# Performance work log

Measured on AMD Instinct MI355X. Metric: run time of the kernel, lower is better.

## Reference

```python
import jax, jax.numpy as jnp
import numpy as np

B, S, N, D = 4, 1024, 16, 512
H, HD = 8, 64
THETA = 10000.0


def setup_inputs() -> dict:
    key = jax.random.key(0)
    k0, k1, k2, k3 = jax.random.split(key, 4)
    x = jax.random.normal(k0, (B, S, N, D), dtype=jnp.float32)
    pos_bias = jax.random.normal(k1, (H, N, N), dtype=jnp.float32)
    W_qkv = jax.random.normal(k2, (D, 3 * H * HD), dtype=jnp.float32) / np.sqrt(D).astype(np.float32)
    W_out = jax.random.normal(k3, (H * HD, D), dtype=jnp.float32) / np.sqrt(H * HD).astype(np.float32)
    # mixed mask (not all True -> no early-return path; not all False -> masking active)
    focus_present_mask = jnp.array([True, False, True, False])
    return {"x": x, "pos_bias": pos_bias, "W_qkv": W_qkv, "W_out": W_out,
            "focus_present_mask": focus_present_mask}


def _rotary_cos_sin(n, d, dtype):
    # rotary-embedding-torch: inv_freq over even indices, each freq repeated twice adjacently
    inv_freq = 1.0 / (THETA ** (jnp.arange(0, d, 2, dtype=jnp.float32) / d))
    freqs = jnp.arange(n, dtype=jnp.float32)[:, None] * inv_freq  # (n, d/2)
    freqs = jnp.repeat(freqs, 2, axis=-1)                          # (n, d)
    return jnp.cos(freqs).astype(dtype), jnp.sin(freqs).astype(dtype)


def _rotate_half(t):
    # pairs (x0, x1) -> (-x1, x0), interleaved layout
    t2 = t.reshape(*t.shape[:-1], t.shape[-1] // 2, 2)
    t2 = jnp.stack([-t2[..., 1], t2[..., 0]], axis=-1)
    return t2.reshape(t.shape)


def reference(x, pos_bias, W_qkv, W_out, focus_present_mask):
    scale = HD ** -0.5
    n = x.shape[-2]
    qkv = x @ W_qkv                                   # (b, s, n, 3*h*hd)
    q, k, v = jnp.split(qkv, 3, axis=-1)

    def to_heads(t):  # (..., n, h*hd) -> (..., h, n, hd)
        return t.reshape(*t.shape[:-1], H, HD).swapaxes(-2, -3)

    q = to_heads(q) * scale
    k = to_heads(k)
    v = to_heads(v)

    cos, sin = _rotary_cos_sin(n, HD, q.dtype)
    q = q * cos + _rotate_half(q) * sin
    k = k * cos + _rotate_half(k) * sin

    sim = jnp.einsum('bshid,bshjd->bshij', q, k)      # (b, s, h, n, n)
    sim = sim + pos_bias                              # broadcast (h, n, n)

    eye = jnp.eye(n, dtype=bool)
    ones = jnp.ones((n, n), dtype=bool)
    mask = jnp.where(focus_present_mask[:, None, None, None, None],
                     eye[None, None, None], ones[None, None, None])
    sim = jnp.where(mask, sim, -jnp.finfo(sim.dtype).max)

    attn = jax.nn.softmax(sim, axis=-1)
    out = jnp.einsum('bshij,bshjd->bshid', attn, v)   # (b, s, h, n, hd)
    out = out.swapaxes(-2, -3).reshape(*x.shape[:-1], H * HD)
    return out @ W_out
```

## Files before the change

kernel.cpp:

```cpp
#include <hip/hip_runtime.h>
#include <cstdint>

#define BB   4
#define SS   1024
#define NTOK 16
#define DD   512
#define HH   8
#define HD   64
#define M_TOTAL (BB * SS * NTOK)
#define QKV_COLS (3 * HH * HD)

typedef unsigned short u16;
typedef short bf16x8 __attribute__((ext_vector_type(8)));
typedef float f32x4 __attribute__((ext_vector_type(4)));

__device__ __forceinline__ float bf2f(u16 u) {
  union { uint32_t i; float f; } x; x.i = ((uint32_t)u) << 16; return x.f;
}
__device__ __forceinline__ u16 f2bf(float f) {
  union { uint32_t i; float f; } x; x.f = f;
  uint32_t i = x.i;
  if ((i & 0x7fffffffu) > 0x7f800000u) return 0x7fc0;
  uint32_t r = (i + 0x7fffu + ((i >> 16) & 1u)) >> 16;
  return (u16)r;
}

__device__ __forceinline__ bool decode_mask(const void* p, int b) {
  uint32_t w0 = *(const uint32_t*)p;
  if (w0 == 0x00010001u) return ((const uint8_t*)p)[b] != 0;
  if (w0 == 0x00003F80u) return ((const u16*)p)[b] != 0;
  if (w0 == 0x3F800000u) return ((const float*)p)[b] != 0.0f;
  return ((const int32_t*)p)[b] != 0;
}

__global__ void sniff_kernel(const u16* __restrict__ x, int* __restrict__ flag) {
  __shared__ int any;
  if (threadIdx.x == 0) any = 0;
  __syncthreads();
  int cnt = 0;
  for (int i = threadIdx.x; i < 8192; i += 256) {
    int e = (x[i] >> 7) & 0xFF;
    if (e >= 141) cnt++;
  }
  if (cnt) atomicOr(&any, 1);
  __syncthreads();
  if (threadIdx.x == 0) *flag = any ? 1 : 0;
}

__global__ void rot_table_kernel(float* __restrict__ cosv, float* __restrict__ sinv) {
  for (int p = threadIdx.x; p < NTOK * 32; p += 256) {
    int n = p >> 5, i = p & 31;
    float ang = (float)n * powf(10000.0f, -(float)(2 * i) / 64.0f);
    cosv[p] = cosf(ang);
    sinv[p] = sinf(ang);
  }
}

__global__ __launch_bounds__(256) void cast_x_kernel(
    const void* __restrict__ src, u16* __restrict__ dst, size_t elem_off,
    const int* __restrict__ flag) {
  size_t i = ((size_t)blockIdx.x * 256 + threadIdx.x) * 4;
  ushort4 o;
  if (*flag) {
    float4 v = *(const float4*)((const float*)src + elem_off + i);
    o.x = f2bf(v.x); o.y = f2bf(v.y); o.z = f2bf(v.z); o.w = f2bf(v.w);
  } else {
    o = *(const ushort4*)((const u16*)src + elem_off + i);
  }
  *(ushort4*)(dst + i) = o;
}

__global__ __launch_bounds__(256) void cast_wt_kernel(
    const void* __restrict__ W, u16* __restrict__ WT, int K, int N,
    const int* __restrict__ flag) {
  size_t idx = (size_t)blockIdx.x * 256 + threadIdx.x;
  int n = (int)(idx / K), k = (int)(idx % K);
  float v = (*flag) ? ((const float*)W)[(size_t)k * N + n]
                    : bf2f(((const u16*)W)[(size_t)k * N + n]);
  WT[idx] = f2bf(v);
}

template <int OUT_F32>
__global__ __launch_bounds__(256) void gemm_mfma_bt(
    const u16* __restrict__ A, const u16* __restrict__ BT, void* __restrict__ Cbase,
    size_t c_elem_off, int M, int N, int K, const int* __restrict__ flag) {
  __shared__ u16 Asl[128 * 32];
  __shared__ u16 Bsl[128 * 32];
  const int tid  = threadIdx.x;
  const int wave = tid >> 6;
  const int lane = tid & 63;
  const int bm = blockIdx.y * 128;
  const int bn = blockIdx.x * 128;
  const int wm = (wave >> 1) * 64;
  const int wn = (wave & 1) * 64;
  const int m_lane = lane & 15;
  const int kgrp   = lane >> 4;

  f32x4 acc[4][4];
#pragma unroll
  for (int r = 0; r < 4; ++r)
#pragma unroll
    for (int c = 0; c < 4; ++c) acc[r][c] = (f32x4){0.f, 0.f, 0.f, 0.f};

  for (int k0 = 0; k0 < K; k0 += 32) {
#pragma unroll
    for (int q = 0; q < 2; ++q) {
      const int idx = q * 256 + tid;
      const int row = idx >> 2;
      const int gc  = (idx & 3) ^ (row & 3);
      const u16* ga = A  + (size_t)(bm + row) * K + k0 + gc * 8;
      const u16* gb = BT + (size_t)(bn + row) * K + k0 + gc * 8;
      u16* la = Asl + (size_t)(q * 256 + wave * 64) * 8;
      u16* lb = Bsl + (size_t)(q * 256 + wave * 64) * 8;
      __builtin_amdgcn_global_load_lds(
          (const __attribute__((address_space(1))) void*)ga,
          (__attribute__((address_space(3))) void*)la, 16, 0, 0);
      __builtin_amdgcn_global_load_lds(
          (const __attribute__((address_space(1))) void*)gb,
          (__attribute__((address_space(3))) void*)lb, 16, 0, 0);
    }
    __syncthreads();

    bf16x8 af[4], bfr[4];
#pragma unroll
    for (int r = 0; r < 4; ++r) {
      const int ra = wm + r * 16 + m_lane;
      af[r] = *(const bf16x8*)(Asl + ra * 32 + ((kgrp ^ (ra & 3)) * 8));
    }
#pragma unroll
    for (int c = 0; c < 4; ++c) {
      const int rb = wn + c * 16 + m_lane;
      bfr[c] = *(const bf16x8*)(Bsl + rb * 32 + ((kgrp ^ (rb & 3)) * 8));
    }
#pragma unroll
    for (int r = 0; r < 4; ++r)
#pragma unroll
      for (int c = 0; c < 4; ++c)
        acc[r][c] = __builtin_amdgcn_mfma_f32_16x16x32_bf16(af[r], bfr[c], acc[r][c], 0, 0, 0);
    __syncthreads();
  }

  const bool f32out = OUT_F32 && (*flag != 0);
#pragma unroll
  for (int r = 0; r < 4; ++r) {
    const int grow0 = bm + wm + r * 16 + kgrp * 4;
#pragma unroll
    for (int c = 0; c < 4; ++c) {
      const int gcol = bn + wn + c * 16 + m_lane;
#pragma unroll
      for (int j = 0; j < 4; ++j) {
        const size_t off = c_elem_off + (size_t)(grow0 + j) * N + gcol;
        if (f32out) ((float*)Cbase)[off] = acc[r][c][j];
        else        ((u16*)Cbase)[off]   = f2bf(acc[r][c][j]);
      }
    }
  }
}

__global__ __launch_bounds__(256) void attn_kernel(
    const u16* __restrict__ qkv, const void* __restrict__ pos_bias,
    const void* __restrict__ maskp, u16* __restrict__ attno, int bs0,
    const float* __restrict__ cosv, const float* __restrict__ sinv,
    const int* __restrict__ flag) {
  __shared__ float lcos[NTOK * 33];
  __shared__ float lsin[NTOK * 33];
  const int tid = threadIdx.x;
  for (int p = tid; p < NTOK * 32; p += 256) {
    int n = p >> 5, i = p & 31;
    lcos[n * 33 + i] = cosv[p];
    lsin[n * 33 + i] = sinv[p];
  }
  __syncthreads();

  const int wave = tid >> 6;
  const int lane = tid & 63;
  const int wid = blockIdx.x * 4 + wave;
  const int bsl = wid >> 3;
  const int h = wid & (HH - 1);
  const int b = (bs0 + bsl) >> 10;
  const int qt = lane & 15;
  const int kg = lane >> 4;

  const u16* rowp = qkv + ((size_t)bsl * NTOK + qt) * QKV_COLS + h * HD;
  float qv[16], kv[16];
#pragma unroll
  for (int hf = 0; hf < 2; ++hf) {
    const bf16x8 uq = *(const bf16x8*)(rowp + hf * 32 + kg * 8);
    const bf16x8 uk = *(const bf16x8*)(rowp + 512 + hf * 32 + kg * 8);
#pragma unroll
    for (int t = 0; t < 8; ++t) {
      qv[hf * 8 + t] = bf2f((u16)uq[t]);
      kv[hf * 8 + t] = bf2f((u16)uk[t]);
    }
  }

  const u16* vbase = qkv + (size_t)bsl * NTOK * QKV_COLS + 1024 + h * HD;
  u16 vraw[32];
#pragma unroll
  for (int mt = 0; mt < 4; ++mt)
#pragma unroll
    for (int t = 0; t < 8; ++t)
      vraw[mt * 8 + t] = (kg < 2)
          ? vbase[(size_t)(kg * 8 + t) * QKV_COLS + mt * 16 + qt]
          : (u16)0;

  bf16x8 qa[2], ka[2];
#pragma unroll
  for (int hf = 0; hf < 2; ++hf) {
#pragma unroll
    for (int t = 0; t < 4; ++t) {
      const int idx = qt * 33 + hf * 16 + kg * 4 + t;
      const float cth = lcos[idx], sth = lsin[idx];
      const int e0 = hf * 8 + 2 * t, e1 = e0 + 1;
      const float q0 = qv[e0], q1 = qv[e1];
      qa[hf][2 * t]     = (short)f2bf((q0 * cth - q1 * sth) * 0.125f);
      qa[hf][2 * t + 1] = (short)f2bf((q1 * cth + q0 * sth) * 0.125f);
      const float k0 = kv[e0], k1 = kv[e1];
      ka[hf][2 * t]     = (short)f2bf(k0 * cth - k1 * sth);
      ka[hf][2 * t + 1] = (short)f2bf(k1 * cth + k0 * sth);
    }
  }

  f32x4 cacc = (f32x4){0.f, 0.f, 0.f, 0.f};
  cacc = __builtin_amdgcn_mfma_f32_16x16x32_bf16(ka[0], qa[0], cacc, 0, 0, 0);
  cacc = __builtin_amdgcn_mfma_f32_16x16x32_bf16(ka[1], qa[1], cacc, 0, 0, 0);

  const bool f32pb = (*flag != 0);
  const bool focus = decode_mask(maskp, b);
  float sv[4];
#pragma unroll
  for (int j = 0; j < 4; ++j) {
    const int kt = kg * 4 + j;
    const size_t pbidx = ((size_t)h * NTOK + qt) * NTOK + kt;
    const float pb = f32pb ? ((const float*)pos_bias)[pbidx]
                           : bf2f(((const u16*)pos_bias)[pbidx]);
    float v = cacc[j] + pb;
    if (focus && (qt != kt)) v = -3.0e38f;
    sv[j] = v;
  }

  float m = fmaxf(fmaxf(sv[0], sv[1]), fmaxf(sv[2], sv[3]));
  m = fmaxf(m, __shfl_xor(m, 16, 64));
  m = fmaxf(m, __shfl_xor(m, 32, 64));
  float pj[4];
  float ssum = 0.f;
#pragma unroll
  for (int j = 0; j < 4; ++j) {
    pj[j] = expf(sv[j] - m);
    ssum += pj[j];
  }
  ssum += __shfl_xor(ssum, 16, 64);
  ssum += __shfl_xor(ssum, 32, 64);
  const float inv = 1.0f / ssum;
#pragma unroll
  for (int j = 0; j < 4; ++j) pj[j] *= inv;

  bf16x8 pfrag;
#pragma unroll
  for (int t = 0; t < 8; ++t) {
    const int src = (lane & 15) + (((kg << 1) + (t >> 2)) << 4);
    const float v = __shfl(pj[t & 3], src & 63, 64);
    pfrag[t] = (kg < 2) ? (short)f2bf(v) : (short)0;
  }

  u16* orow = attno + ((size_t)bsl * NTOK + qt) * (HH * HD) + h * HD;
#pragma unroll
  for (int mt = 0; mt < 4; ++mt) {
    bf16x8 vfrag;
#pragma unroll
    for (int t = 0; t < 8; ++t) vfrag[t] = (short)vraw[mt * 8 + t];
    f32x4 o = (f32x4){0.f, 0.f, 0.f, 0.f};
    o = __builtin_amdgcn_mfma_f32_16x16x32_bf16(vfrag, pfrag, o, 0, 0, 0);
    ushort4 uo;
    uo.x = f2bf(o[0]); uo.y = f2bf(o[1]); uo.z = f2bf(o[2]); uo.w = f2bf(o[3]);
    *(ushort4*)(orow + mt * 16 + kg * 4) = uo;
  }
}

extern "C" void kernel_launch(void* const* d_in, const int* in_sizes, int n_in,
                              void* d_out, int out_size, void* d_ws, size_t ws_size,
                              hipStream_t stream) {
  const void* x_raw    = d_in[0];
  const void* pos_bias = d_in[1];
  const void* W_qkv    = d_in[2];
  const void* W_out    = d_in[3];
  const void* maskp    = d_in[4];

  char* ws = (char*)d_ws;
  int*   flag = (int*)ws;
  float* cosv = (float*)(ws + 256);
  float* sinv = cosv + NTOK * 32;
  u16* WqT = (u16*)(ws + 256 + 4096);
  u16* WoT = WqT + (size_t)QKV_COLS * DD;
  u16* scratch = WoT + (size_t)DD * DD;
  const size_t fixed = 256 + 4096 + (size_t)QKV_COLS * DD * 2 + (size_t)DD * DD * 2;
  const size_t ws_avail = (ws_size > fixed) ? ws_size - fixed : 0;

  const size_t per_row = 5120;
  int chunk_rows = M_TOTAL;
  while ((size_t)chunk_rows * per_row > ws_avail && chunk_rows > 128) chunk_rows >>= 1;
  const int nchunks = M_TOTAL / chunk_rows;

  u16* xb    = scratch;
  u16* qkv   = xb  + (size_t)chunk_rows * DD;
  u16* attno = qkv + (size_t)chunk_rows * QKV_COLS;

  sniff_kernel<<<1, 256, 0, stream>>>((const u16*)x_raw, flag);
  rot_table_kernel<<<1, 256, 0, stream>>>(cosv, sinv);
  cast_wt_kernel<<<(QKV_COLS * DD) / 256, 256, 0, stream>>>(W_qkv, WqT, DD, QKV_COLS, flag);
  cast_wt_kernel<<<(DD * DD) / 256, 256, 0, stream>>>(W_out, WoT, DD, DD, flag);

  for (int c = 0; c < nchunks; ++c) {
    const int bs0 = c * (chunk_rows / NTOK);
    const size_t eoff = (size_t)c * chunk_rows * DD;

    cast_x_kernel<<<(int)(((size_t)chunk_rows * DD) / 1024), 256, 0, stream>>>(
        x_raw, xb, eoff, flag);

    {
      dim3 grid(QKV_COLS / 128, chunk_rows / 128);
      gemm_mfma_bt<0><<<grid, 256, 0, stream>>>(xb, WqT, (void*)qkv, 0,
                                                chunk_rows, QKV_COLS, DD, flag);
    }
    {
      dim3 grid(((chunk_rows / NTOK) * HH) / 4);
      attn_kernel<<<grid, 256, 0, stream>>>(qkv, pos_bias, maskp, attno, bs0,
                                            cosv, sinv, flag);
    }
    {
      dim3 grid(DD / 128, chunk_rows / 128);
      gemm_mfma_bt<1><<<grid, 256, 0, stream>>>(attno, WoT, d_out, eoff,
                                                chunk_rows, DD, DD, flag);
    }
  }
}
```

Measured before the change: 538.6 us.

## Replace GEMM with 256x256 double-buffered 8-wave kernel and XCD-aware tile swizzle

Replaces the 128x128 single-buffered GEMM with a 256x256 tile, 512-thread kernel. Global-to-LDS loads for the next K tile are double-buffered and interleaved with MFMA phases using explicit vmcnt waits, barriers and setprio. Work-group IDs are remapped so neighbouring tiles land on the same XCD. The cost targeted is exposed load latency and low reuse per tile. In exchange it uses more LDS and registers, launches fewer blocks (possible tail effects for the N=512 output GEMM), and drops the LDS XOR swizzle, which may bring back bank conflicts.

```diff
diff --git a/kernel.cpp b/kernel.cpp
--- a/kernel.cpp
+++ b/kernel.cpp
@@ -81,77 +81,118 @@
 }
 
 template <int OUT_F32>
-__global__ __launch_bounds__(256) void gemm_mfma_bt(
+__global__ __launch_bounds__(512, 2) void gemm_mfma_bt256(
     const u16* __restrict__ A, const u16* __restrict__ BT, void* __restrict__ Cbase,
     size_t c_elem_off, int M, int N, int K, const int* __restrict__ flag) {
-  __shared__ u16 Asl[128 * 32];
-  __shared__ u16 Bsl[128 * 32];
+  __shared__ u16 As[2][2][256 * 32];
+  __shared__ u16 Bs[2][2][256 * 32];
   const int tid  = threadIdx.x;
   const int wave = tid >> 6;
   const int lane = tid & 63;
-  const int bm = blockIdx.y * 128;
-  const int bn = blockIdx.x * 128;
-  const int wm = (wave >> 1) * 64;
-  const int wn = (wave & 1) * 64;
+  const int wr = wave >> 2;
+  const int wc = wave & 3;
   const int m_lane = lane & 15;
   const int kgrp   = lane >> 4;
 
-  f32x4 acc[4][4];
-#pragma unroll
-  for (int r = 0; r < 4; ++r)
-#pragma unroll
-    for (int c = 0; c < 4; ++c) acc[r][c] = (f32x4){0.f, 0.f, 0.f, 0.f};
-
-  for (int k0 = 0; k0 < K; k0 += 32) {
-#pragma unroll
-    for (int q = 0; q < 2; ++q) {
-      const int idx = q * 256 + tid;
-      const int row = idx >> 2;
-      const int gc  = (idx & 3) ^ (row & 3);
-      const u16* ga = A  + (size_t)(bm + row) * K + k0 + gc * 8;
-      const u16* gb = BT + (size_t)(bn + row) * K + k0 + gc * 8;
-      u16* la = Asl + (size_t)(q * 256 + wave * 64) * 8;
-      u16* lb = Bsl + (size_t)(q * 256 + wave * 64) * 8;
+  const int nwg = (int)gridDim.x;
+  const int bid = (int)blockIdx.x;
+  const int q8 = nwg >> 3, r8 = nwg & 7;
+  const int xcd = bid & 7;
+  const int swz = ((xcd < r8) ? xcd * (q8 + 1) : r8 * (q8 + 1) + (xcd - r8) * q8)
+                  + (bid >> 3);
+  const int nbn = N >> 8;
+  const int bm = (swz / nbn) << 8;
+  const int bn = (swz % nbn) << 8;
+
+  const u16* Ag = A  + (size_t)bm * K;
+  const u16* Bg = BT + (size_t)bn * K;
+
+  f32x4 acc[8][4];
+#pragma unroll
+  for (int m = 0; m < 8; ++m)
+#pragma unroll
+    for (int n = 0; n < 4; ++n) acc[m][n] = (f32x4){0.f, 0.f, 0.f, 0.f};
+
+  auto stage = [&](const u16* gbase, int tile, int kh, u16* lbase) {
+#pragma unroll
+    for (int l = 0; l < 2; ++l) {
+      const int slot = l * 512 + tid;
+      const u16* ga = gbase + (size_t)(slot >> 2) * K + tile * 64 + kh * 32
+                      + (slot & 3) * 8;
+      u16* la = lbase + (size_t)(l * 512 + wave * 64) * 8;
       __builtin_amdgcn_global_load_lds(
           (const __attribute__((address_space(1))) void*)ga,
           (__attribute__((address_space(3))) void*)la, 16, 0, 0);
-      __builtin_amdgcn_global_load_lds(
-          (const __attribute__((address_space(1))) void*)gb,
-          (__attribute__((address_space(3))) void*)lb, 16, 0, 0);
-    }
-    __syncthreads();
-
+    }
+  };
+
+  const int nt = K >> 6;
+
+  stage(Ag, 0, 0, As[0][0]);
+  stage(Bg, 0, 0, Bs[0][0]);
+  stage(Ag, 0, 1, As[0][1]);
+  stage(Bg, 0, 1, Bs[0][1]);
+  asm volatile("s_waitcnt vmcnt(4)" ::: "memory");
+  __builtin_amdgcn_s_barrier();
+  __builtin_amdgcn_sched_barrier(0);
+
+  for (int u = 0; u < nt; ++u) {
+    const int b = u & 1, nb = b ^ 1;
+    const bool pf = (u + 1 < nt);
     bf16x8 af[4], bfr[4];
 #pragma unroll
-    for (int r = 0; r < 4; ++r) {
-      const int ra = wm + r * 16 + m_lane;
-      af[r] = *(const bf16x8*)(Asl + ra * 32 + ((kgrp ^ (ra & 3)) * 8));
-    }
-#pragma unroll
-    for (int c = 0; c < 4; ++c) {
-      const int rb = wn + c * 16 + m_lane;
-      bfr[c] = *(const bf16x8*)(Bsl + rb * 32 + ((kgrp ^ (rb & 3)) * 8));
-    }
-#pragma unroll
-    for (int r = 0; r < 4; ++r)
-#pragma unroll
-      for (int c = 0; c < 4; ++c)
-        acc[r][c] = __builtin_amdgcn_mfma_f32_16x16x32_bf16(af[r], bfr[c], acc[r][c], 0, 0, 0);
-    __syncthreads();
+    for (int ks = 0; ks < 2; ++ks) {
+#pragma unroll
+      for (int m = 0; m < 4; ++m)
+        af[m] = *(const bf16x8*)&As[b][ks][(wr * 128 + m * 16 + m_lane) * 32 + kgrp * 8];
+#pragma unroll
+      for (int n = 0; n < 4; ++n)
+        bfr[n] = *(const bf16x8*)&Bs[b][ks][(wc * 64 + n * 16 + m_lane) * 32 + kgrp * 8];
+      if (pf) stage(Ag, u + 1, ks, As[nb][ks]);
+      __builtin_amdgcn_s_barrier();
+      __builtin_amdgcn_sched_barrier(0);
+      __builtin_amdgcn_s_setprio(1);
+#pragma unroll
+      for (int m = 0; m < 4; ++m)
+#pragma unroll
+        for (int n = 0; n < 4; ++n)
+          acc[m][n] = __builtin_amdgcn_mfma_f32_16x16x32_bf16(af[m], bfr[n], acc[m][n], 0, 0, 0);
+      __builtin_amdgcn_s_setprio(0);
+      __builtin_amdgcn_s_barrier();
+      __builtin_amdgcn_sched_barrier(0);
+
+#pragma unroll
+      for (int m = 0; m < 4; ++m)
+        af[m] = *(const bf16x8*)&As[b][ks][(wr * 128 + (m + 4) * 16 + m_lane) * 32 + kgrp * 8];
+      if (pf) stage(Bg, u + 1, ks, Bs[nb][ks]);
+      if (pf) asm volatile("s_waitcnt vmcnt(4)" ::: "memory");
+      else    asm volatile("s_waitcnt vmcnt(0)" ::: "memory");
+      __builtin_amdgcn_s_barrier();
+      __builtin_amdgcn_sched_barrier(0);
+      __builtin_amdgcn_s_setprio(1);
+#pragma unroll
+      for (int m = 0; m < 4; ++m)
+#pragma unroll
+        for (int n = 0; n < 4; ++n)
+          acc[m + 4][n] = __builtin_amdgcn_mfma_f32_16x16x32_bf16(af[m], bfr[n], acc[m + 4][n], 0, 0, 0);
+      __builtin_amdgcn_s_setprio(0);
+      __builtin_amdgcn_s_barrier();
+      __builtin_amdgcn_sched_barrier(0);
+    }
   }
 
   const bool f32out = OUT_F32 && (*flag != 0);
 #pragma unroll
-  for (int r = 0; r < 4; ++r) {
-    const int grow0 = bm + wm + r * 16 + kgrp * 4;
-#pragma unroll
-    for (int c = 0; c < 4; ++c) {
-      const int gcol = bn + wn + c * 16 + m_lane;
+  for (int m = 0; m < 8; ++m) {
+    const int grow0 = bm + wr * 128 + m * 16 + kgrp * 4;
+#pragma unroll
+    for (int n = 0; n < 4; ++n) {
+      const int gcol = bn + wc * 64 + n * 16 + m_lane;
 #pragma unroll
       for (int j = 0; j < 4; ++j) {
         const size_t off = c_elem_off + (size_t)(grow0 + j) * N + gcol;
-        if (f32out) ((float*)Cbase)[off] = acc[r][c][j];
-        else        ((u16*)Cbase)[off]   = f2bf(acc[r][c][j]);
+        if (f32out) ((float*)Cbase)[off] = acc[m][n][j];
+        else        ((u16*)Cbase)[off]   = f2bf(acc[m][n][j]);
       }
     }
   }
@@ -298,7 +339,7 @@
 
   const size_t per_row = 5120;
   int chunk_rows = M_TOTAL;
-  while ((size_t)chunk_rows * per_row > ws_avail && chunk_rows > 128) chunk_rows >>= 1;
+  while ((size_t)chunk_rows * per_row > ws_avail && chunk_rows > 256) chunk_rows >>= 1;
   const int nchunks = M_TOTAL / chunk_rows;
 
   u16* xb    = scratch;
@@ -318,9 +359,9 @@
         x_raw, xb, eoff, flag);
 
     {
-      dim3 grid(QKV_COLS / 128, chunk_rows / 128);
-      gemm_mfma_bt<0><<<grid, 256, 0, stream>>>(xb, WqT, (void*)qkv, 0,
-                                                chunk_rows, QKV_COLS, DD, flag);
+      dim3 grid((chunk_rows / 256) * (QKV_COLS / 256));
+      gemm_mfma_bt256<0><<<grid, 512, 0, stream>>>(xb, WqT, (void*)qkv, 0,
+                                                   chunk_rows, QKV_COLS, DD, flag);
     }
     {
       dim3 grid(((chunk_rows / NTOK) * HH) / 4);
@@ -328,9 +369,9 @@
                                             cosv, sinv, flag);
     }
     {
-      dim3 grid(DD / 128, chunk_rows / 128);
-      gemm_mfma_bt<1><<<grid, 256, 0, stream>>>(attno, WoT, d_out, eoff,
-                                                chunk_rows, DD, DD, flag);
-    }
-  }
-}
+      dim3 grid((chunk_rows / 256) * (DD / 256));
+      gemm_mfma_bt256<1><<<grid, 512, 0, stream>>>(attno, WoT, d_out, eoff,
+                                                   chunk_rows, DD, DD, flag);
+    }
+  }
+}
```

Result: faster. 524.1 us (-2.7%).
